# Kernel optimization log

Measured on AMD Instinct MI355X. Metric: run time of the kernel, lower is better.

## Reference

```python
import jax, jax.numpy as jnp
import numpy as np

PSP_SIZES = (1, 3, 6, 8)  # KV length S = 1 + 9 + 36 + 64 = 110
BN_EPS = 1e-5


def conv1x1(x, W, b):
    # x: [B,C,H,W], W: [O,C], b: [O] -> [B,O,H,W]
    return jnp.einsum('bchw,oc->bohw', x, W) + b[None, :, None, None]


def psp(f):
    # f: [B,C,H,W] -> [B,C,S]; H,W divisible by all sizes so adaptive pool == block mean
    B, C, H, W = f.shape
    priors = []
    for s in PSP_SIZES:
        p = f.reshape(B, C, s, H // s, s, W // s).mean(axis=(3, 5))  # [B,C,s,s]
        priors.append(p.reshape(B, C, s * s))
    return jnp.concatenate(priors, axis=-1)  # [B,C,S]


def setup_inputs() -> dict:
    key = jax.random.key(0)
    ks = jax.random.split(key, 8)
    B, C, H, W = 8, 512, 72, 72
    Kc, Vc = 256, 256
    return {
        'x': jax.random.normal(ks[0], (B, C, H, W), jnp.float32),
        'Wk': jax.random.normal(ks[1], (Kc, C), jnp.float32) * (1.0 / np.sqrt(C)),
        'bk': jax.random.normal(ks[2], (Kc,), jnp.float32) * 0.01,
        'gamma': jnp.ones((Kc,), jnp.float32),
        'beta': jnp.zeros((Kc,), jnp.float32),
        'rmean': jnp.zeros((Kc,), jnp.float32),
        'rvar': jax.random.uniform(ks[3], (Kc,), jnp.float32, 0.5, 1.5),
        'Wv': jax.random.normal(ks[4], (Vc, C), jnp.float32) * (1.0 / np.sqrt(C)),
        'bv': jax.random.normal(ks[5], (Vc,), jnp.float32) * 0.01,
        'Ww': jax.random.normal(ks[6], (C, Vc), jnp.float32) * (1.0 / np.sqrt(Vc)),
        'bw': jnp.zeros((C,), jnp.float32),
    }


def reference(x, Wk, bk, gamma, beta, rmean, rvar, Wv, bv, Ww, bw):
    B, C, H, W = x.shape
    Kc = Wk.shape[0]
    Vc = Wv.shape[0]
    # f_value: conv1x1, then PSP -> value [B,S,Vc]
    value = psp(conv1x1(x, Wv, bv)).transpose(0, 2, 1)
    # f_key == f_query: conv1x1 + BN(inference) + ReLU
    k = conv1x1(x, Wk, bk)
    inv = gamma / jnp.sqrt(rvar + BN_EPS)
    k = jax.nn.relu(k * inv[None, :, None, None] + (beta - rmean * inv)[None, :, None, None])
    query = k.reshape(B, Kc, H * W).transpose(0, 2, 1)  # [B,HW,Kc]
    keyt = psp(k)  # [B,Kc,S]
    sim = jnp.einsum('bnk,bks->bns', query, keyt) * (Kc ** -0.5)
    sim = jax.nn.softmax(sim, axis=-1)
    context = jnp.einsum('bns,bsv->bnv', sim, value)  # [B,HW,Vc]
    context = context.transpose(0, 2, 1).reshape(B, Vc, H, W)
    return conv1x1(context, Ww, bw)
```

## Files before the change

kernel.cpp:

```cpp
#include <hip/hip_runtime.h>
#include <hip/hip_bf16.h>

#define HW    5184
#define WIDTH 72
#define CIN   512
#define KC    256
#define VC    256
#define NS    110
#define NSP   112
#define SPV   128
#define BATCH 8

typedef unsigned short u16;
typedef unsigned int   u32;
typedef __attribute__((ext_vector_type(8))) short bf16x8;
typedef __attribute__((ext_vector_type(4))) float f32x4;

typedef const __attribute__((address_space(1))) u32* gp_t;
typedef __attribute__((address_space(3))) u32* lp_t;

__device__ __forceinline__ u32 f2bf1(float f) {
    u32 u = __float_as_uint(f);
    return (u + 0x7FFFu + ((u >> 16) & 1u)) >> 16;
}
__device__ __forceinline__ u32 pack2(float a, float b) {
    return f2bf1(a) | (f2bf1(b) << 16);
}
__device__ __forceinline__ float bf2f(u16 h) {
    return __uint_as_float((u32)h << 16);
}

__global__ void prep_kernel(const float* __restrict__ bk, const float* __restrict__ gamma,
                            const float* __restrict__ beta, const float* __restrict__ rmean,
                            const float* __restrict__ rvar, float* __restrict__ inv_out,
                            float* __restrict__ bc_out) {
    int i = threadIdx.x;
    float inv = gamma[i] * rsqrtf(rvar[i] + 1e-5f);
    inv_out[i] = inv;
    bc_out[i]  = bk[i] * inv + beta[i] - rmean[i] * inv;
}

__global__ __launch_bounds__(256) void cvt_w_kernel(
    const float* __restrict__ Wk, const float* __restrict__ Ww, const float* __restrict__ Wv,
    u16* __restrict__ Wkbf, u16* __restrict__ Wwbf, u16* __restrict__ Wvbf)
{
    int j = (blockIdx.x * 256 + threadIdx.x) * 4;
    const float* s; u16* d;
    if (j < KC * CIN)          { s = Wk; d = Wkbf; }
    else if (j < 2 * KC * CIN) { j -= KC * CIN;     s = Ww; d = Wwbf; }
    else                       { j -= 2 * KC * CIN; s = Wv; d = Wvbf; }
    float4 v = *(const float4*)&s[j];
    uint2 u;
    u.x = pack2(v.x, v.y);
    u.y = pack2(v.z, v.w);
    *(uint2*)&d[j] = u;
}

__global__ __launch_bounds__(256) void transpose_pool_kernel(
    const float* __restrict__ in, u16* __restrict__ xT, float* __restrict__ rpx)
{
    const int y  = blockIdx.x;
    const int c0 = blockIdx.y * 64;
    const int b  = blockIdx.z;
    const int t  = threadIdx.x;
    __shared__ float tile[64][73];
    const float* src = in + ((size_t)b * CIN + c0) * HW + (size_t)y * WIDTH;
    for (int idx = t; idx < 64 * 18; idx += 256) {
        const int cc = idx / 18, seg = idx - cc * 18;
        float4 v = *(const float4*)(src + (size_t)cc * HW + seg * 4);
        tile[cc][seg * 4 + 0] = v.x;
        tile[cc][seg * 4 + 1] = v.y;
        tile[cc][seg * 4 + 2] = v.z;
        tile[cc][seg * 4 + 3] = v.w;
    }
    __syncthreads();
    {
        const int kp  = (t & 31) * 2;
        const int nl0 = t >> 5;
        u16* dst = xT + ((size_t)b * HW + (size_t)y * WIDTH) * CIN + c0 + kp;
#pragma unroll
        for (int j = 0; j < 9; j++) {
            const int px = nl0 + j * 8;
            u32 u = pack2(tile[kp][px], tile[kp + 1][px]);
            *(u32*)&dst[(size_t)px * CIN] = u;
        }
    }
    if (t < 64) {
        float s9[8]  = {0.f, 0.f, 0.f, 0.f, 0.f, 0.f, 0.f, 0.f};
        float s12[6] = {0.f, 0.f, 0.f, 0.f, 0.f, 0.f};
#pragma unroll
        for (int x = 0; x < 72; x++) {
            float v = tile[t][x];
            s9[x / 9] += v;
            s12[x / 12] += v;
        }
        float* dst = rpx + (((size_t)b * 72 + y) * 15) * CIN + c0 + t;
        float tot = 0.f;
#pragma unroll
        for (int g = 0; g < 8; g++) dst[(size_t)g * CIN] = s9[g];
#pragma unroll
        for (int g = 0; g < 6; g++) { dst[(size_t)(8 + g) * CIN] = s12[g]; tot += s12[g]; }
        dst[(size_t)14 * CIN] = tot;
    }
}

__global__ __launch_bounds__(256) void binpool_px_kernel(
    const float* __restrict__ rpx, u16* __restrict__ pxb)
{
    const int s = blockIdx.x;
    const int b = blockIdx.y;
    const int t = threadIdx.x;
    u16* ob = pxb + ((size_t)b * SPV + s) * CIN;
    if (s >= NS) { ob[t] = 0; ob[t + 256] = 0; return; }
#pragma unroll
    for (int h = 0; h < 2; h++) {
        const int c = t + h * 256;
        const float* rpb = rpx + (size_t)b * 72 * 15 * CIN + c;
        float sum = 0.f, scl = 0.f;
        if (s == 0) {
#pragma unroll 8
            for (int y = 0; y < 72; y++) sum += rpb[((size_t)y * 15 + 14) * CIN];
            scl = 1.f / 5184.f;
        } else if (s < 10) {
            const int tt = s - 1, gy = tt / 3, gx = tt - gy * 3;
#pragma unroll 8
            for (int i = 0; i < 24; i++) {
                const int y = gy * 24 + i;
                sum += rpb[((size_t)y * 15 + 8 + 2 * gx) * CIN]
                     + rpb[((size_t)y * 15 + 9 + 2 * gx) * CIN];
            }
            scl = 1.f / 576.f;
        } else if (s < 46) {
            const int tt = s - 10, gy = tt / 6, gx = tt - gy * 6;
#pragma unroll
            for (int i = 0; i < 12; i++) {
                const int y = gy * 12 + i;
                sum += rpb[((size_t)y * 15 + 8 + gx) * CIN];
            }
            scl = 1.f / 144.f;
        } else {
            const int tt = s - 46, gy = tt >> 3, gx = tt & 7;
#pragma unroll
            for (int i = 0; i < 9; i++) {
                const int y = gy * 9 + i;
                sum += rpb[((size_t)y * 15 + gx) * CIN];
            }
            scl = 1.f / 81.f;
        }
        ob[c] = (u16)f2bf1(sum * scl);
    }
}

__global__ __launch_bounds__(256) void gemm_nt_bf16(
    const u16* __restrict__ A, const u16* __restrict__ B, float* __restrict__ C,
    u16* __restrict__ Ct,
    int M, int N, int K, int nbx, int nby,
    const float* __restrict__ scale, const float* __restrict__ bias, int relu)
{
    const int tot = nbx * nby * BATCH;
    const int q = tot >> 3, r = tot & 7;
    const int xcd = blockIdx.x & 7;
    const int wg  = (xcd < r ? xcd * (q + 1) : r * (q + 1) + (xcd - r) * q) + (blockIdx.x >> 3);
    const int mb_ = wg % nby;
    const int nb_ = (wg / nby) % nbx;
    const int z   = wg / (nby * nbx);

    const int n0 = nb_ * 128;
    const int m0 = mb_ * 128;
    const size_t boff = (size_t)z * N * K;
    const size_t coff = (size_t)z * M * N;
    const int tid  = threadIdx.x;
    const int wid  = tid >> 6;
    const int lane = tid & 63;

    __shared__ __align__(16) u16 As[3][4][128][8];
    __shared__ __align__(16) u16 Bs[3][4][128][8];

    const int kg0  = (wid & 1) * 2;
    const int half = (wid >> 1) * 64;

    const u16* gA = A + (size_t)(m0 + half + lane) * K + kg0 * 8;
    int nIdx = n0 + half + lane;
    if (nIdx > N - 1) nIdx = N - 1;
    const u16* gB = B + boff + (size_t)nIdx * K + kg0 * 8;

    const int wm  = (wid >> 1) * 64;
    const int wn  = (wid & 1) * 64;
    const int l16 = lane & 15;
    const int lq  = lane >> 4;

    f32x4 acc[4][4];
#pragma unroll
    for (int mi = 0; mi < 4; mi++)
#pragma unroll
        for (int ni = 0; ni < 4; ni++)
            acc[mi][ni] = (f32x4){0.f, 0.f, 0.f, 0.f};

#define STAGE(d, kk)                                                                              \
    __builtin_amdgcn_global_load_lds((gp_t)(gA + (kk)),     (lp_t)&As[d][kg0][half][0], 16, 0, 0);\
    __builtin_amdgcn_global_load_lds((gp_t)(gA + (kk) + 8), (lp_t)&As[d][kg0+1][half][0],16, 0, 0);\
    __builtin_amdgcn_global_load_lds((gp_t)(gB + (kk)),     (lp_t)&Bs[d][kg0][half][0], 16, 0, 0);\
    __builtin_amdgcn_global_load_lds((gp_t)(gB + (kk) + 8), (lp_t)&Bs[d][kg0+1][half][0],16, 0, 0);

    const int NT = K >> 5;
    STAGE(0, 0)
    STAGE(1, 32)

    int cur = 0;
    for (int t = 0; t < NT; ++t) {
        if (t + 1 < NT) { asm volatile("s_waitcnt vmcnt(4)" ::: "memory"); }
        else            { asm volatile("s_waitcnt vmcnt(0)" ::: "memory"); }
        __builtin_amdgcn_s_barrier();
        __builtin_amdgcn_sched_barrier(0);

        if (t + 2 < NT) {
            int nb = cur + 2; if (nb >= 3) nb -= 3;
            STAGE(nb, (t + 2) * 32)
        }

        bf16x8 af[4], bf[4];
#pragma unroll
        for (int i = 0; i < 4; i++) {
            af[i] = *(const bf16x8*)&As[cur][lq][wm + i * 16 + l16][0];
            bf[i] = *(const bf16x8*)&Bs[cur][lq][wn + i * 16 + l16][0];
        }
        __builtin_amdgcn_s_setprio(1);
#pragma unroll
        for (int mi = 0; mi < 4; mi++)
#pragma unroll
            for (int ni = 0; ni < 4; ni++)
                acc[mi][ni] = __builtin_amdgcn_mfma_f32_16x16x32_bf16(
                    af[mi], bf[ni], acc[mi][ni], 0, 0, 0);
        __builtin_amdgcn_s_setprio(0);

        cur = (cur == 2) ? 0 : cur + 1;
    }
#undef STAGE

#pragma unroll
    for (int mi = 0; mi < 4; mi++) {
        const int mb = m0 + wm + mi * 16 + lq * 4;
        float sc[4], bi[4];
#pragma unroll
        for (int r2 = 0; r2 < 4; r2++) {
            sc[r2] = scale ? scale[mb + r2] : 1.0f;
            bi[r2] = bias  ? bias[mb + r2]  : 0.0f;
        }
#pragma unroll
        for (int ni = 0; ni < 4; ni++) {
            const int n = n0 + wn + ni * 16 + l16;
            if (n < N) {
                float v[4];
#pragma unroll
                for (int r2 = 0; r2 < 4; r2++) {
                    v[r2] = acc[mi][ni][r2] * sc[r2] + bi[r2];
                    if (relu) v[r2] = fmaxf(v[r2], 0.f);
                }
                if (C) {
#pragma unroll
                    for (int r2 = 0; r2 < 4; r2++)
                        C[coff + (size_t)(mb + r2) * N + n] = v[r2];
                }
                if (Ct) {
                    uint2 u;
                    u.x = pack2(v[0], v[1]);
                    u.y = pack2(v[2], v[3]);
                    *(uint2*)&Ct[(size_t)z * N * M + (size_t)n * M + mb] = u;
                }
            }
        }
    }
}

__global__ __launch_bounds__(256) void rowpool_k_kernel(
    const u16* __restrict__ kT, float* __restrict__ rp)
{
    const int y = blockIdx.x;
    const int b = blockIdx.y;
    const int c = threadIdx.x;
    const u16* src = kT + ((size_t)b * HW + (size_t)y * WIDTH) * KC + c;
    float s9[8]  = {0.f, 0.f, 0.f, 0.f, 0.f, 0.f, 0.f, 0.f};
    float s12[6] = {0.f, 0.f, 0.f, 0.f, 0.f, 0.f};
#pragma unroll
    for (int x = 0; x < 72; x++) {
        float v = bf2f(src[(size_t)x * KC]);
        s9[x / 9] += v;
        s12[x / 12] += v;
    }
    float* dst = rp + (((size_t)b * 72 + y) * 15) * KC + c;
    float tot = 0.f;
#pragma unroll
    for (int g = 0; g < 8; g++) dst[(size_t)g * KC] = s9[g];
#pragma unroll
    for (int g = 0; g < 6; g++) { dst[(size_t)(8 + g) * KC] = s12[g]; tot += s12[g]; }
    dst[(size_t)14 * KC] = tot;
}

__global__ __launch_bounds__(256) void binpool_k_kernel(
    const float* __restrict__ rp, u16* __restrict__ keytb)
{
    const int s = blockIdx.x;
    const int b = blockIdx.y;
    const int c = threadIdx.x;
    char* ob = (char*)keytb + (size_t)b * NSP * KC * 2;
    float sum = 0.f, scl = 0.f;
    const float* rpb = rp + (size_t)b * 72 * 15 * KC + c;
    if (s < NS) {
        if (s == 0) {
#pragma unroll 8
            for (int y = 0; y < 72; y++) sum += rpb[((size_t)y * 15 + 14) * KC];
            scl = 1.f / 5184.f;
        } else if (s < 10) {
            const int t = s - 1, gy = t / 3, gx = t - gy * 3;
#pragma unroll 8
            for (int i = 0; i < 24; i++) {
                const int y = gy * 24 + i;
                sum += rpb[((size_t)y * 15 + 8 + 2 * gx) * KC]
                     + rpb[((size_t)y * 15 + 9 + 2 * gx) * KC];
            }
            scl = 1.f / 576.f;
        } else if (s < 46) {
            const int t = s - 10, gy = t / 6, gx = t - gy * 6;
#pragma unroll
            for (int i = 0; i < 12; i++) {
                const int y = gy * 12 + i;
                sum += rpb[((size_t)y * 15 + 8 + gx) * KC];
            }
            scl = 1.f / 144.f;
        } else {
            const int t = s - 46, gy = t >> 3, gx = t & 7;
#pragma unroll
            for (int i = 0; i < 9; i++) {
                const int y = gy * 9 + i;
                sum += rpb[((size_t)y * 15 + gx) * KC];
            }
            scl = 1.f / 81.f;
        }
    }
    const int byte = s * 512 + ((c * 2) ^ ((s & 7) << 4));
    *(u16*)(ob + byte) = (s < NS) ? (u16)f2bf1(sum * scl) : (u16)0;
}

__global__ __launch_bounds__(256) void value_mfma_kernel(
    const u16* __restrict__ A, const u16* __restrict__ Bp,
    const float* __restrict__ bv, u16* __restrict__ valT)
{
    const int m0 = blockIdx.x * 128;
    const int b  = blockIdx.y;
    const int tid  = threadIdx.x;
    const int wid  = tid >> 6;
    const int lane = tid & 63;

    __shared__ __align__(16) u16 As[4][128][8];
    __shared__ __align__(16) u16 Bs[4][128][8];

    const int kg0  = (wid & 1) * 2;
    const int half = (wid >> 1) * 64;

    const u16* gA = A + (size_t)(m0 + half + lane) * CIN + kg0 * 8;
    const u16* gB = Bp + (size_t)b * SPV * CIN + (size_t)(half + lane) * CIN + kg0 * 8;

    lp_t lA0 = (lp_t)&As[kg0][half][0];
    lp_t lA1 = (lp_t)&As[kg0 + 1][half][0];
    lp_t lB0 = (lp_t)&Bs[kg0][half][0];
    lp_t lB1 = (lp_t)&Bs[kg0 + 1][half][0];

    const int wm  = (wid >> 1) * 64;
    const int wn  = (wid & 1) * 64;
    const int l16 = lane & 15;
    const int lq  = lane >> 4;

    f32x4 acc[4][4];
#pragma unroll
    for (int mi = 0; mi < 4; mi++)
#pragma unroll
        for (int ni = 0; ni < 4; ni++)
            acc[mi][ni] = (f32x4){0.f, 0.f, 0.f, 0.f};

    for (int k0 = 0; k0 < CIN; k0 += 32) {
        __builtin_amdgcn_global_load_lds((gp_t)(gA + k0),     lA0, 16, 0, 0);
        __builtin_amdgcn_global_load_lds((gp_t)(gA + k0 + 8), lA1, 16, 0, 0);
        __builtin_amdgcn_global_load_lds((gp_t)(gB + k0),     lB0, 16, 0, 0);
        __builtin_amdgcn_global_load_lds((gp_t)(gB + k0 + 8), lB1, 16, 0, 0);
        __syncthreads();

        bf16x8 af[4], bf[4];
#pragma unroll
        for (int i = 0; i < 4; i++) {
            af[i] = *(const bf16x8*)&As[lq][wm + i * 16 + l16][0];
            bf[i] = *(const bf16x8*)&Bs[lq][wn + i * 16 + l16][0];
        }
#pragma unroll
        for (int mi = 0; mi < 4; mi++)
#pragma unroll
            for (int ni = 0; ni < 4; ni++)
                acc[mi][ni] = __builtin_amdgcn_mfma_f32_16x16x32_bf16(
                    af[mi], bf[ni], acc[mi][ni], 0, 0, 0);
        __syncthreads();
    }

    char* vb = (char*)valT + (size_t)b * VC * SPV * 2;
#pragma unroll
    for (int mi = 0; mi < 4; mi++) {
        const int mb = m0 + wm + mi * 16 + lq * 4;
        float bi[4];
#pragma unroll
        for (int r = 0; r < 4; r++) bi[r] = bv[mb + r];
#pragma unroll
        for (int ni = 0; ni < 4; ni++) {
            const int n = wn + ni * 16 + l16;
#pragma unroll
            for (int r = 0; r < 4; r++) {
                const int v = mb + r;
                const int byte = v * 256 + ((n * 2) ^ ((v & 7) << 4));
                *(u16*)(vb + byte) = (u16)f2bf1(acc[mi][ni][r] + bi[r]);
            }
        }
    }
}

__global__ __launch_bounds__(256, 3) void attn_mfma_kernel(
    const u16* __restrict__ qT, const u16* __restrict__ keyt,
    const u16* __restrict__ valT, const u16* __restrict__ Wwb,
    const float* __restrict__ bw, float* __restrict__ out)
{
    const int b    = blockIdx.y;
    const int tid  = threadIdx.x;
    const int wid  = tid >> 6;
    const int lane = tid & 63;
    const int l16  = lane & 15;
    const int lq   = lane >> 4;
    const int nblk = blockIdx.x * 64;
    const int px0  = nblk + wid * 16;

    __shared__ __align__(16) u16 SM[24576];
    char* base = (char*)SM;
    const int POFF = 32768;

    const char* gk = (const char*)keyt + (size_t)b * (NSP * KC * 2);
    const char* gv = (const char*)valT + (size_t)b * (VC * SPV * 2);

#pragma unroll
    for (int i = 0; i < 8; i++) {
        const int o = (wid * 8 + i) * 1024;
        __builtin_amdgcn_global_load_lds((gp_t)(gk + o + lane * 16), (lp_t)(base + o), 16, 0, 0);
    }

    const u16* qrow = qT + ((size_t)b * HW + px0 + l16) * KC + lq * 8;
    bf16x8 aq[8];
#pragma unroll
    for (int ks = 0; ks < 8; ks++) aq[ks] = *(const bf16x8*)(qrow + ks * 32);

    __syncthreads();

    f32x4 acc[7];
#pragma unroll
    for (int ni = 0; ni < 7; ni++) acc[ni] = (f32x4){0.f, 0.f, 0.f, 0.f};
#pragma unroll
    for (int ks = 0; ks < 8; ks++) {
#pragma unroll
        for (int ni = 0; ni < 4; ni++) {
            const int s = ni * 16 + l16;
            const int byte = s * 512 + ((ks * 64 + lq * 16) ^ ((s & 7) << 4));
            bf16x8 bk = *(const bf16x8*)(base + byte);
            acc[ni] = __builtin_amdgcn_mfma_f32_16x16x32_bf16(aq[ks], bk, acc[ni], 0, 0, 0);
        }
    }
    __syncthreads();

#pragma unroll
    for (int i = 0; i < 6; i++) {
        const int o = (wid * 6 + i) * 1024;
        __builtin_amdgcn_global_load_lds((gp_t)(gk + 32768 + o + lane * 16), (lp_t)(base + o), 16, 0, 0);
    }
    __syncthreads();

#pragma unroll
    for (int ks = 0; ks < 8; ks++) {
#pragma unroll
        for (int ni = 4; ni < 7; ni++) {
            const int s = ni * 16 + l16;
            const int srow = s - 64;
            const int byte = srow * 512 + ((ks * 64 + lq * 16) ^ ((srow & 7) << 4));
            bf16x8 bk = *(const bf16x8*)(base + byte);
            acc[ni] = __builtin_amdgcn_mfma_f32_16x16x32_bf16(aq[ks], bk, acc[ni], 0, 0, 0);
        }
    }
    if (l16 >= 14) acc[6] = (f32x4){-1e30f, -1e30f, -1e30f, -1e30f};
    __syncthreads();

#pragma unroll
    for (int i = 0; i < 8; i++) {
        const int o = (wid * 8 + i) * 1024;
        __builtin_amdgcn_global_load_lds((gp_t)(gv + o + lane * 16), (lp_t)(base + o), 16, 0, 0);
    }

    float mx[4], sm[4], rn[4];
#pragma unroll
    for (int r = 0; r < 4; r++) {
        float m = acc[0][r];
#pragma unroll
        for (int ni = 1; ni < 7; ni++) m = fmaxf(m, acc[ni][r]);
        m = fmaxf(m, __shfl_xor(m, 1));
        m = fmaxf(m, __shfl_xor(m, 2));
        m = fmaxf(m, __shfl_xor(m, 4));
        m = fmaxf(m, __shfl_xor(m, 8));
        mx[r] = m * 0.0625f;
        sm[r] = 0.f;
    }

    const int prow = wid * 16 + 4 * lq;
#pragma unroll
    for (int ni = 0; ni < 7; ni++) {
#pragma unroll
        for (int r = 0; r < 4; r++) {
            float p = __expf(acc[ni][r] * 0.0625f - mx[r]);
            sm[r] += p;
            const int row = prow + r;
            const int byte = POFF + row * 256 + (((ni * 16 + l16) * 2) ^ ((row & 7) << 4));
            *(u16*)(base + byte) = (u16)f2bf1(p);
        }
    }
    if (l16 < 2) {
#pragma unroll
        for (int r = 0; r < 4; r++) {
            const int row = prow + r;
            const int byte = POFF + row * 256 + ((224 + l16 * 16) ^ ((row & 7) << 4));
            *(bf16x8*)(base + byte) = (bf16x8){0, 0, 0, 0, 0, 0, 0, 0};
        }
    }
#pragma unroll
    for (int r = 0; r < 4; r++) {
        float s = sm[r];
        s += __shfl_xor(s, 1);
        s += __shfl_xor(s, 2);
        s += __shfl_xor(s, 4);
        s += __shfl_xor(s, 8);
        rn[r] = 1.f / s;
    }
    __syncthreads();

    f32x4 acc2[16];
#pragma unroll
    for (int ni = 0; ni < 16; ni++) acc2[ni] = (f32x4){0.f, 0.f, 0.f, 0.f};
    const int arow = wid * 16 + l16;
    const int aswz = (arow & 7) << 4;
#pragma unroll
    for (int ks = 0; ks < 4; ks++) {
        const int pbyte = POFF + arow * 256 + ((ks * 64 + lq * 16) ^ aswz);
        bf16x8 pa = *(const bf16x8*)(base + pbyte);
#pragma unroll
        for (int ni = 0; ni < 8; ni++) {
            const int v = ni * 16 + l16;
            const int vbyte = v * 256 + ((ks * 64 + lq * 16) ^ ((v & 7) << 4));
            bf16x8 bvv = *(const bf16x8*)(base + vbyte);
            acc2[ni] = __builtin_amdgcn_mfma_f32_16x16x32_bf16(pa, bvv, acc2[ni], 0, 0, 0);
        }
    }
    __syncthreads();

#pragma unroll
    for (int i = 0; i < 8; i++) {
        const int o = (wid * 8 + i) * 1024;
        __builtin_amdgcn_global_load_lds((gp_t)(gv + 32768 + o + lane * 16), (lp_t)(base + o), 16, 0, 0);
    }
    __syncthreads();

#pragma unroll
    for (int ks = 0; ks < 4; ks++) {
        const int pbyte = POFF + arow * 256 + ((ks * 64 + lq * 16) ^ aswz);
        bf16x8 pa = *(const bf16x8*)(base + pbyte);
#pragma unroll
        for (int ni = 8; ni < 16; ni++) {
            const int vrow = (ni - 8) * 16 + l16;
            const int vbyte = vrow * 256 + ((ks * 64 + lq * 16) ^ ((vrow & 7) << 4));
            bf16x8 bvv = *(const bf16x8*)(base + vbyte);
            acc2[ni] = __builtin_amdgcn_mfma_f32_16x16x32_bf16(pa, bvv, acc2[ni], 0, 0, 0);
        }
    }
    __syncthreads();

#pragma unroll
    for (int ni = 0; ni < 16; ni++) {
#pragma unroll
        for (int r = 0; r < 4; r++) {
            const int row = prow + r;
            const int v = ni * 16 + l16;
            const int byte = row * 512 + ((v * 2) ^ ((row & 7) << 4));
            *(u16*)(base + byte) = (u16)f2bf1(acc2[ni][r] * rn[r]);
        }
    }
    __syncthreads();

    const int wc0 = wid * 128;
    float* outb = out + (size_t)b * CIN * HW + nblk;
    char* scr = base + POFF + wid * 4096;

#pragma unroll
    for (int ch = 0; ch < 2; ch++) {
        f32x4 accg[4][4];
#pragma unroll
        for (int pi = 0; pi < 4; pi++)
#pragma unroll
            for (int cj = 0; cj < 4; cj++)
                accg[pi][cj] = (f32x4){0.f, 0.f, 0.f, 0.f};

        const u16* wwbase = Wwb + (size_t)(wc0 + ch * 64 + l16) * VC + lq * 8;
#pragma unroll
        for (int ks = 0; ks < 8; ks++) {
            bf16x8 af[4];
#pragma unroll
            for (int pi = 0; pi < 4; pi++) {
                const int px = pi * 16 + l16;
                const int byte = px * 512 + ((ks * 64 + lq * 16) ^ ((px & 7) << 4));
                af[pi] = *(const bf16x8*)(base + byte);
            }
            bf16x8 bfr[4];
#pragma unroll
            for (int cj = 0; cj < 4; cj++)
                bfr[cj] = *(const bf16x8*)(wwbase + (size_t)cj * 16 * VC + ks * 32);
#pragma unroll
            for (int pi = 0; pi < 4; pi++)
#pragma unroll
                for (int cj = 0; cj < 4; cj++)
                    accg[pi][cj] = __builtin_amdgcn_mfma_f32_16x16x32_bf16(
                        af[pi], bfr[cj], accg[pi][cj], 0, 0, 0);
        }

#pragma unroll
        for (int cj = 0; cj < 4; cj++) {
            const int cl = l16;
            const int swz = (cl & 7) << 5;
#pragma unroll
            for (int pi = 0; pi < 4; pi++)
#pragma unroll
                for (int r = 0; r < 4; r++) {
                    const int px = pi * 16 + 4 * lq + r;
                    *(float*)(scr + cl * 256 + ((px * 4) ^ swz)) = accg[pi][cj][r];
                }
#pragma unroll
            for (int cr = 0; cr < 4; cr++) {
                const int cl2 = cr * 4 + lq;
                const int swz2 = (cl2 & 7) << 5;
                float4 vv = *(const float4*)(scr + cl2 * 256 + ((l16 * 16) ^ swz2));
                const int c = wc0 + ch * 64 + cj * 16 + cl2;
                const float bb = bw[c];
                vv.x += bb; vv.y += bb; vv.z += bb; vv.w += bb;
                *(float4*)&outb[(size_t)c * HW + l16 * 4] = vv;
            }
        }
    }
}

extern "C" void kernel_launch(void* const* d_in, const int* in_sizes, int n_in,
                              void* d_out, int out_size, void* d_ws, size_t ws_size,
                              hipStream_t stream)
{
    const float* x     = (const float*)d_in[0];
    const float* Wk    = (const float*)d_in[1];
    const float* bk    = (const float*)d_in[2];
    const float* gamma = (const float*)d_in[3];
    const float* beta  = (const float*)d_in[4];
    const float* rmean = (const float*)d_in[5];
    const float* rvar  = (const float*)d_in[6];
    const float* Wv    = (const float*)d_in[7];
    const float* bv    = (const float*)d_in[8];
    const float* Ww    = (const float*)d_in[9];
    const float* bw    = (const float*)d_in[10];
    float* out = (float*)d_out;

    float* ws    = (float*)d_ws;
    float* rpk   = ws;
    float* rpx   = rpk + (size_t)BATCH * 72 * 15 * KC;
    u16*   xT    = (u16*)(rpx + (size_t)BATCH * 72 * 15 * CIN);
    u16*   kT    = xT + (size_t)BATCH * HW * CIN;
    u16*   pxb   = kT + (size_t)BATCH * HW * KC;
    u16*   keytb = pxb + (size_t)BATCH * SPV * CIN;
    u16*   valT  = keytb + (size_t)BATCH * NSP * KC;
    u16*   Wkbf  = valT + (size_t)BATCH * VC * SPV;
    u16*   Wwbf  = Wkbf + (size_t)KC * CIN;
    u16*   Wvbf  = Wwbf + (size_t)CIN * VC;
    float* inv   = (float*)(Wvbf + (size_t)KC * CIN);
    float* bc    = inv + 256;

    prep_kernel<<<1, 256, 0, stream>>>(bk, gamma, beta, rmean, rvar, inv, bc);
    cvt_w_kernel<<<384, 256, 0, stream>>>(Wk, Ww, Wv, Wkbf, Wwbf, Wvbf);
    transpose_pool_kernel<<<dim3(72, CIN / 64, BATCH), 256, 0, stream>>>(x, xT, rpx);
    binpool_px_kernel<<<dim3(SPV, BATCH), 256, 0, stream>>>(rpx, pxb);
    {
        const int nbx = (HW + 127) / 128, nby = KC / 128;
        gemm_nt_bf16<<<nbx * nby * BATCH, 256, 0, stream>>>(
            Wkbf, xT, nullptr, kT, KC, HW, CIN, nbx, nby, inv, bc, 1);
    }
    rowpool_k_kernel<<<dim3(72, BATCH), 256, 0, stream>>>(kT, rpk);
    binpool_k_kernel<<<dim3(NSP, BATCH), 256, 0, stream>>>(rpk, keytb);
    value_mfma_kernel<<<dim3(2, BATCH), 256, 0, stream>>>(Wvbf, pxb, bv, valT);
    attn_mfma_kernel<<<dim3(HW / 64, BATCH), 256, 0, stream>>>(
        kT, keytb, valT, Wwbf, bw, out);
}
```

Before: 160.6 us.

## Halve attention block to 32 pixels with 2 waves and smaller LDS staging

```diff
diff --git a/kernel.cpp b/kernel.cpp
--- a/kernel.cpp
+++ b/kernel.cpp
@@ -419,7 +419,7 @@
     }
 }
 
-__global__ __launch_bounds__(256, 3) void attn_mfma_kernel(
+__global__ __launch_bounds__(128, 3) void attn_mfma_kernel(
     const u16* __restrict__ qT, const u16* __restrict__ keyt,
     const u16* __restrict__ valT, const u16* __restrict__ Wwb,
     const float* __restrict__ bw, float* __restrict__ out)
@@ -430,19 +430,19 @@
     const int lane = tid & 63;
     const int l16  = lane & 15;
     const int lq   = lane >> 4;
-    const int nblk = blockIdx.x * 64;
+    const int nblk = blockIdx.x * 32;
     const int px0  = nblk + wid * 16;
 
-    __shared__ __align__(16) u16 SM[24576];
+    __shared__ __align__(16) u16 SM[16384];
     char* base = (char*)SM;
-    const int POFF = 32768;
+    const int POFF = 24576;
 
     const char* gk = (const char*)keyt + (size_t)b * (NSP * KC * 2);
     const char* gv = (const char*)valT + (size_t)b * (VC * SPV * 2);
 
 #pragma unroll
-    for (int i = 0; i < 8; i++) {
-        const int o = (wid * 8 + i) * 1024;
+    for (int i = 0; i < 12; i++) {
+        const int o = (wid * 12 + i) * 1024;
         __builtin_amdgcn_global_load_lds((gp_t)(gk + o + lane * 16), (lp_t)(base + o), 16, 0, 0);
     }
 
@@ -456,10 +456,11 @@
     f32x4 acc[7];
 #pragma unroll
     for (int ni = 0; ni < 7; ni++) acc[ni] = (f32x4){0.f, 0.f, 0.f, 0.f};
+
 #pragma unroll
     for (int ks = 0; ks < 8; ks++) {
 #pragma unroll
-        for (int ni = 0; ni < 4; ni++) {
+        for (int ni = 0; ni < 3; ni++) {
             const int s = ni * 16 + l16;
             const int byte = s * 512 + ((ks * 64 + lq * 16) ^ ((s & 7) << 4));
             bf16x8 bk = *(const bf16x8*)(base + byte);
@@ -469,29 +470,45 @@
     __syncthreads();
 
 #pragma unroll
-    for (int i = 0; i < 6; i++) {
-        const int o = (wid * 6 + i) * 1024;
-        __builtin_amdgcn_global_load_lds((gp_t)(gk + 32768 + o + lane * 16), (lp_t)(base + o), 16, 0, 0);
+    for (int i = 0; i < 12; i++) {
+        const int o = (wid * 12 + i) * 1024;
+        __builtin_amdgcn_global_load_lds((gp_t)(gk + 24576 + o + lane * 16), (lp_t)(base + o), 16, 0, 0);
     }
     __syncthreads();
 
 #pragma unroll
     for (int ks = 0; ks < 8; ks++) {
 #pragma unroll
-        for (int ni = 4; ni < 7; ni++) {
-            const int s = ni * 16 + l16;
-            const int srow = s - 64;
-            const int byte = srow * 512 + ((ks * 64 + lq * 16) ^ ((srow & 7) << 4));
+        for (int ni = 3; ni < 6; ni++) {
+            const int row = ni * 16 + l16 - 48;
+            const int byte = row * 512 + ((ks * 64 + lq * 16) ^ ((row & 7) << 4));
             bf16x8 bk = *(const bf16x8*)(base + byte);
             acc[ni] = __builtin_amdgcn_mfma_f32_16x16x32_bf16(aq[ks], bk, acc[ni], 0, 0, 0);
         }
     }
+    __syncthreads();
+
+#pragma unroll
+    for (int i = 0; i < 4; i++) {
+        const int o = (wid * 4 + i) * 1024;
+        __builtin_amdgcn_global_load_lds((gp_t)(gk + 49152 + o + lane * 16), (lp_t)(base + o), 16, 0, 0);
+    }
+    __syncthreads();
+
+#pragma unroll
+    for (int ks = 0; ks < 8; ks++) {
+        const int row = 96 + l16 - 96 + (6 * 16 - 96);
+        const int byte = l16 * 512 + ((ks * 64 + lq * 16) ^ ((l16 & 7) << 4));
+        bf16x8 bk = *(const bf16x8*)(base + byte);
+        acc[6] = __builtin_amdgcn_mfma_f32_16x16x32_bf16(aq[ks], bk, acc[6], 0, 0, 0);
+        (void)row;
+    }
     if (l16 >= 14) acc[6] = (f32x4){-1e30f, -1e30f, -1e30f, -1e30f};
     __syncthreads();
 
 #pragma unroll
-    for (int i = 0; i < 8; i++) {
-        const int o = (wid * 8 + i) * 1024;
+    for (int i = 0; i < 12; i++) {
+        const int o = (wid * 12 + i) * 1024;
         __builtin_amdgcn_global_load_lds((gp_t)(gv + o + lane * 16), (lp_t)(base + o), 16, 0, 0);
     }
 
@@ -545,12 +562,13 @@
     for (int ni = 0; ni < 16; ni++) acc2[ni] = (f32x4){0.f, 0.f, 0.f, 0.f};
     const int arow = wid * 16 + l16;
     const int aswz = (arow & 7) << 4;
+
 #pragma unroll
     for (int ks = 0; ks < 4; ks++) {
         const int pbyte = POFF + arow * 256 + ((ks * 64 + lq * 16) ^ aswz);
         bf16x8 pa = *(const bf16x8*)(base + pbyte);
 #pragma unroll
-        for (int ni = 0; ni < 8; ni++) {
+        for (int ni = 0; ni < 6; ni++) {
             const int v = ni * 16 + l16;
             const int vbyte = v * 256 + ((ks * 64 + lq * 16) ^ ((v & 7) << 4));
             bf16x8 bvv = *(const bf16x8*)(base + vbyte);
@@ -560,9 +578,9 @@
     __syncthreads();
 
 #pragma unroll
-    for (int i = 0; i < 8; i++) {
-        const int o = (wid * 8 + i) * 1024;
-        __builtin_amdgcn_global_load_lds((gp_t)(gv + 32768 + o + lane * 16), (lp_t)(base + o), 16, 0, 0);
+    for (int i = 0; i < 12; i++) {
+        const int o = (wid * 12 + i) * 1024;
+        __builtin_amdgcn_global_load_lds((gp_t)(gv + 24576 + o + lane * 16), (lp_t)(base + o), 16, 0, 0);
     }
     __syncthreads();
 
@@ -571,9 +589,30 @@
         const int pbyte = POFF + arow * 256 + ((ks * 64 + lq * 16) ^ aswz);
         bf16x8 pa = *(const bf16x8*)(base + pbyte);
 #pragma unroll
-        for (int ni = 8; ni < 16; ni++) {
-            const int vrow = (ni - 8) * 16 + l16;
-            const int vbyte = vrow * 256 + ((ks * 64 + lq * 16) ^ ((vrow & 7) << 4));
+        for (int ni = 6; ni < 12; ni++) {
+            const int row = ni * 16 + l16 - 96;
+            const int vbyte = row * 256 + ((ks * 64 + lq * 16) ^ ((row & 7) << 4));
+            bf16x8 bvv = *(const bf16x8*)(base + vbyte);
+            acc2[ni] = __builtin_amdgcn_mfma_f32_16x16x32_bf16(pa, bvv, acc2[ni], 0, 0, 0);
+        }
+    }
+    __syncthreads();
+
+#pragma unroll
+    for (int i = 0; i < 8; i++) {
+        const int o = (wid * 8 + i) * 1024;
+        __builtin_amdgcn_global_load_lds((gp_t)(gv + 49152 + o + lane * 16), (lp_t)(base + o), 16, 0, 0);
+    }
+    __syncthreads();
+
+#pragma unroll
+    for (int ks = 0; ks < 4; ks++) {
+        const int pbyte = POFF + arow * 256 + ((ks * 64 + lq * 16) ^ aswz);
+        bf16x8 pa = *(const bf16x8*)(base + pbyte);
+#pragma unroll
+        for (int ni = 12; ni < 16; ni++) {
+            const int row = ni * 16 + l16 - 192;
+            const int vbyte = row * 256 + ((ks * 64 + lq * 16) ^ ((row & 7) << 4));
             bf16x8 bvv = *(const bf16x8*)(base + vbyte);
             acc2[ni] = __builtin_amdgcn_mfma_f32_16x16x32_bf16(pa, bvv, acc2[ni], 0, 0, 0);
         }
@@ -592,15 +631,15 @@
     }
     __syncthreads();
 
-    const int wc0 = wid * 128;
+    const int wc0 = wid * 256;
     float* outb = out + (size_t)b * CIN * HW + nblk;
     char* scr = base + POFF + wid * 4096;
 
 #pragma unroll
-    for (int ch = 0; ch < 2; ch++) {
-        f32x4 accg[4][4];
-#pragma unroll
-        for (int pi = 0; pi < 4; pi++)
+    for (int ch = 0; ch < 4; ch++) {
+        f32x4 accg[2][4];
+#pragma unroll
+        for (int pi = 0; pi < 2; pi++)
 #pragma unroll
             for (int cj = 0; cj < 4; cj++)
                 accg[pi][cj] = (f32x4){0.f, 0.f, 0.f, 0.f};
@@ -608,9 +647,9 @@
         const u16* wwbase = Wwb + (size_t)(wc0 + ch * 64 + l16) * VC + lq * 8;
 #pragma unroll
         for (int ks = 0; ks < 8; ks++) {
-            bf16x8 af[4];
-#pragma unroll
-            for (int pi = 0; pi < 4; pi++) {
+            bf16x8 af[2];
+#pragma unroll
+            for (int pi = 0; pi < 2; pi++) {
                 const int px = pi * 16 + l16;
                 const int byte = px * 512 + ((ks * 64 + lq * 16) ^ ((px & 7) << 4));
                 af[pi] = *(const bf16x8*)(base + byte);
@@ -620,7 +659,7 @@
             for (int cj = 0; cj < 4; cj++)
                 bfr[cj] = *(const bf16x8*)(wwbase + (size_t)cj * 16 * VC + ks * 32);
 #pragma unroll
-            for (int pi = 0; pi < 4; pi++)
+            for (int pi = 0; pi < 2; pi++)
 #pragma unroll
                 for (int cj = 0; cj < 4; cj++)
                     accg[pi][cj] = __builtin_amdgcn_mfma_f32_16x16x32_bf16(
@@ -628,25 +667,27 @@
         }
 
 #pragma unroll
-        for (int cj = 0; cj < 4; cj++) {
-            const int cl = l16;
-            const int swz = (cl & 7) << 5;
-#pragma unroll
-            for (int pi = 0; pi < 4; pi++)
-#pragma unroll
-                for (int r = 0; r < 4; r++) {
-                    const int px = pi * 16 + 4 * lq + r;
-                    *(float*)(scr + cl * 256 + ((px * 4) ^ swz)) = accg[pi][cj][r];
+        for (int h = 0; h < 2; h++) {
+#pragma unroll
+            for (int cjh = 0; cjh < 2; cjh++) {
+                const int cj = h * 2 + cjh;
+                const int cl = cjh * 16 + l16;
+                const int swz = (cl & 7) << 4;
+#pragma unroll
+                for (int pi = 0; pi < 2; pi++) {
+                    const int pq = (pi * 16 + 4 * lq) * 4;
+                    *(f32x4*)(scr + cl * 128 + (pq ^ swz)) = accg[pi][cj];
                 }
-#pragma unroll
-            for (int cr = 0; cr < 4; cr++) {
-                const int cl2 = cr * 4 + lq;
-                const int swz2 = (cl2 & 7) << 5;
-                float4 vv = *(const float4*)(scr + cl2 * 256 + ((l16 * 16) ^ swz2));
-                const int c = wc0 + ch * 64 + cj * 16 + cl2;
+            }
+#pragma unroll
+            for (int it = 0; it < 4; it++) {
+                const int row = it * 8 + (lane >> 3);
+                const int swz = (row & 7) << 4;
+                float4 vv = *(const float4*)(scr + row * 128 + (((lane & 7) * 16) ^ swz));
+                const int c = wc0 + ch * 64 + h * 32 + row;
                 const float bb = bw[c];
                 vv.x += bb; vv.y += bb; vv.z += bb; vv.w += bb;
-                *(float4*)&outb[(size_t)c * HW + l16 * 4] = vv;
+                *(float4*)&outb[(size_t)c * HW + (lane & 7) * 4] = vv;
             }
         }
     }
@@ -695,6 +736,6 @@
     rowpool_k_kernel<<<dim3(72, BATCH), 256, 0, stream>>>(kT, rpk);
     binpool_k_kernel<<<dim3(NSP, BATCH), 256, 0, stream>>>(rpk, keytb);
     value_mfma_kernel<<<dim3(2, BATCH), 256, 0, stream>>>(Wvbf, pxb, bv, valT);
-    attn_mfma_kernel<<<dim3(HW / 64, BATCH), 256, 0, stream>>>(
+    attn_mfma_kernel<<<dim3(HW / 32, BATCH), 128, 0, stream>>>(
         kT, keytb, valT, Wwbf, bw, out);
 }
```

Result: slower. 196.3 us (+22.2%).
